# Kernel tuning notes

Measured on AMD Instinct MI355X. Metric: run time of the kernel, lower is better.

The kernel has to match this reference:

```python
import jax, jax.numpy as jnp
import numpy as np

B, L, D, K = 16, 2048, 768, 32
NEG = jnp.float32(-1e30)

def setup_inputs() -> dict:
    key = jax.random.key(0)
    k1, k2, k3, k4 = jax.random.split(key, 4)
    token_hidden = jax.random.normal(k1, (B, L, D), dtype=jnp.float32)
    attention_mask = jnp.ones((B, L), dtype=jnp.float32)
    # ragged spans: sorted boundaries -> contiguous, possibly-empty spans
    bounds = jnp.sort(jax.random.randint(k2, (B, K + 1), 0, L), axis=-1)
    span_starts = bounds[:, :-1].astype(jnp.int32)   # [B, K]
    span_ends = bounds[:, 1:].astype(jnp.int32)      # [B, K]
    w_pool = jax.random.normal(k3, (D,), dtype=jnp.float32) * 0.02
    b_pool = jax.random.normal(k4, (1,), dtype=jnp.float32) * 0.02
    return {"token_hidden": token_hidden, "attention_mask": attention_mask,
            "span_starts": span_starts, "span_ends": span_ends,
            "w_pool": w_pool, "b_pool": b_pool}

def reference(token_hidden, attention_mask, span_starts, span_ends, w_pool, b_pool):
    # sent_pool(vecs): scores per token, shared across spans  -> [B, L]
    scores = jnp.einsum('bld,d->bl', token_hidden, w_pool) + b_pool[0]
    pos = jnp.arange(token_hidden.shape[1], dtype=jnp.int32)  # [L]
    # span membership mask [B, K, L]; empty / out-of-range spans -> all False
    span_mask = ((pos[None, None, :] >= span_starts[:, :, None]) &
                 (pos[None, None, :] < span_ends[:, :, None]) &
                 (attention_mask[:, None, :] >= 0.5))
    logits = jnp.where(span_mask, scores[:, None, :], NEG)  # [B, K, L]
    m = jnp.max(logits, axis=-1, keepdims=True)
    e = jnp.exp(logits - m) * span_mask                      # stable masked softmax
    s = jnp.sum(e, axis=-1, keepdims=True)
    w = e / jnp.maximum(s, jnp.float32(1e-30))               # zero rows for empty spans
    H = jnp.einsum('bkl,bld->bkd', w, token_hidden)          # [B, K, D]
    sent_mask = jnp.any(span_mask, axis=-1).astype(jnp.float32)  # [B, K]
    return H, sent_mask
```

## Files before the change

### kernel.cpp

```cpp
#include <hip/hip_runtime.h>

#define BB 16
#define LL 2048
#define DD 768
#define KK 32
#define NEGI -1e30f

__global__ __launch_bounds__(256) void scores_k(
    const float* __restrict__ th,
    const float* __restrict__ attn,
    const float* __restrict__ wp,
    const float* __restrict__ bp,
    float* __restrict__ scores) {
  const int lane = threadIdx.x & 63;
  const int wave = threadIdx.x >> 6;
  const int token = (blockIdx.x << 2) + wave;

  const float4* row = (const float4*)(th + (size_t)token * DD);
  const float4* wr  = (const float4*)wp;

  float4 a0 = row[lane], a1 = row[lane + 64], a2 = row[lane + 128];
  float4 w0 = wr[lane],  w1 = wr[lane + 64],  w2 = wr[lane + 128];

  float acc = 0.f;
  acc = fmaf(a0.x, w0.x, acc); acc = fmaf(a0.y, w0.y, acc);
  acc = fmaf(a0.z, w0.z, acc); acc = fmaf(a0.w, w0.w, acc);
  acc = fmaf(a1.x, w1.x, acc); acc = fmaf(a1.y, w1.y, acc);
  acc = fmaf(a1.z, w1.z, acc); acc = fmaf(a1.w, w1.w, acc);
  acc = fmaf(a2.x, w2.x, acc); acc = fmaf(a2.y, w2.y, acc);
  acc = fmaf(a2.z, w2.z, acc); acc = fmaf(a2.w, w2.w, acc);

  #pragma unroll
  for (int o = 32; o > 0; o >>= 1) acc += __shfl_xor(acc, o, 64);

  if (lane == 0) {
    float s = acc + bp[0];
    scores[token] = (attn[token] >= 0.5f) ? s : NEGI;
  }
}

__global__ __launch_bounds__(64) void pool2_k(
    const float* __restrict__ th,
    const float* __restrict__ scores,
    const int* __restrict__ sps,
    const int* __restrict__ spe,
    float* __restrict__ Hout,
    float* __restrict__ sent) {
  const int bk = blockIdx.x;
  const int chunk = blockIdx.y;
  const int b = bk >> 5;
  const int lane = threadIdx.x;

  __shared__ float lw[LL];

  int s0 = min(max(sps[bk], 0), LL);
  int e0 = min(max(spe[bk], 0), LL);

  const float* sc = scores + (size_t)b * LL;

  float m = NEGI;
  for (int l = s0 + lane; l < e0; l += 64) m = fmaxf(m, sc[l]);
  #pragma unroll
  for (int o = 32; o > 0; o >>= 1) m = fmaxf(m, __shfl_xor(m, o, 64));

  float ss = 0.f;
  for (int l = s0 + lane; l < e0; l += 64) {
    float v = sc[l];
    ss += (v > -1e29f) ? __expf(v - m) : 0.f;
  }
  #pragma unroll
  for (int o = 32; o > 0; o >>= 1) ss += __shfl_xor(ss, o, 64);

  const float inv = (ss > 0.f) ? (1.0f / ss) : 0.f;

  for (int l = s0 + lane; l < e0; l += 64) {
    float v = sc[l];
    lw[l - s0] = (v > -1e29f) ? (__expf(v - m) * inv) : 0.f;
  }
  __syncthreads();

  const float4* base = (const float4*)(th + (size_t)b * LL * DD + chunk * 256) + lane;
  float4 acc = make_float4(0.f, 0.f, 0.f, 0.f);
  #pragma unroll 8
  for (int l = s0; l < e0; ++l) {
    const float w = lw[l - s0];
    float4 t = base[(size_t)l * (DD / 4)];
    acc.x = fmaf(w, t.x, acc.x);
    acc.y = fmaf(w, t.y, acc.y);
    acc.z = fmaf(w, t.z, acc.z);
    acc.w = fmaf(w, t.w, acc.w);
  }

  float4* o = (float4*)(Hout + (size_t)bk * DD + chunk * 256) + lane;
  *o = acc;

  if (chunk == 0 && lane == 0) sent[bk] = (ss > 0.f) ? 1.0f : 0.0f;
}

extern "C" void kernel_launch(void* const* d_in, const int* in_sizes, int n_in,
                              void* d_out, int out_size, void* d_ws, size_t ws_size,
                              hipStream_t stream) {
  const float* th   = (const float*)d_in[0];
  const float* attn = (const float*)d_in[1];
  const int*   sps  = (const int*)d_in[2];
  const int*   spe  = (const int*)d_in[3];
  const float* wp   = (const float*)d_in[4];
  const float* bp   = (const float*)d_in[5];

  float* Hout = (float*)d_out;
  float* sent = Hout + (size_t)BB * KK * DD;

  float* scores = (float*)d_ws;

  scores_k<<<dim3((BB * LL) / 4), dim3(256), 0, stream>>>(th, attn, wp, bp, scores);
  pool2_k<<<dim3(BB * KK, 3), dim3(64), 0, stream>>>(th, scores, sps, spe, Hout, sent);
}
```

Measured before the change: 174.5 us.

## Fuse score computation and span pooling into one online-softmax kernel

Merges the scoring kernel and the pooling kernel into a single per-span kernel. Sixteen waves each stream span rows, compute the dot-product score on the fly and keep an online-softmax running max, sum and weighted accumulator. The per-wave partials are then merged through shared memory. This removes the separate full pass over token_hidden to compute scores, plus the second launch and the workspace round trip. In exchange there are extra exp and rescale ops per token, only 512 blocks of 1024 threads, and load imbalance across uneven span lengths. The bias is dropped, which is valid because softmax is shift-invariant.

```diff
diff --git a/kernel.cpp b/kernel.cpp
--- a/kernel.cpp
+++ b/kernel.cpp
@@ -5,96 +5,94 @@
 #define DD 768
 #define KK 32
 #define NEGI -1e30f
+#define NW 16
 
-__global__ __launch_bounds__(256) void scores_k(
+__global__ __launch_bounds__(1024) void span_pool_k(
     const float* __restrict__ th,
     const float* __restrict__ attn,
-    const float* __restrict__ wp,
-    const float* __restrict__ bp,
-    float* __restrict__ scores) {
-  const int lane = threadIdx.x & 63;
-  const int wave = threadIdx.x >> 6;
-  const int token = (blockIdx.x << 2) + wave;
-
-  const float4* row = (const float4*)(th + (size_t)token * DD);
-  const float4* wr  = (const float4*)wp;
-
-  float4 a0 = row[lane], a1 = row[lane + 64], a2 = row[lane + 128];
-  float4 w0 = wr[lane],  w1 = wr[lane + 64],  w2 = wr[lane + 128];
-
-  float acc = 0.f;
-  acc = fmaf(a0.x, w0.x, acc); acc = fmaf(a0.y, w0.y, acc);
-  acc = fmaf(a0.z, w0.z, acc); acc = fmaf(a0.w, w0.w, acc);
-  acc = fmaf(a1.x, w1.x, acc); acc = fmaf(a1.y, w1.y, acc);
-  acc = fmaf(a1.z, w1.z, acc); acc = fmaf(a1.w, w1.w, acc);
-  acc = fmaf(a2.x, w2.x, acc); acc = fmaf(a2.y, w2.y, acc);
-  acc = fmaf(a2.z, w2.z, acc); acc = fmaf(a2.w, w2.w, acc);
-
-  #pragma unroll
-  for (int o = 32; o > 0; o >>= 1) acc += __shfl_xor(acc, o, 64);
-
-  if (lane == 0) {
-    float s = acc + bp[0];
-    scores[token] = (attn[token] >= 0.5f) ? s : NEGI;
-  }
-}
-
-__global__ __launch_bounds__(64) void pool2_k(
-    const float* __restrict__ th,
-    const float* __restrict__ scores,
     const int* __restrict__ sps,
     const int* __restrict__ spe,
+    const float* __restrict__ wp,
     float* __restrict__ Hout,
     float* __restrict__ sent) {
   const int bk = blockIdx.x;
-  const int chunk = blockIdx.y;
   const int b = bk >> 5;
-  const int lane = threadIdx.x;
+  const int lane = threadIdx.x & 63;
+  const int wave = threadIdx.x >> 6;
 
-  __shared__ float lw[LL];
+  __shared__ float sacc[NW][DD];
+  __shared__ float sm[NW], ssm[NW];
 
   int s0 = min(max(sps[bk], 0), LL);
   int e0 = min(max(spe[bk], 0), LL);
 
-  const float* sc = scores + (size_t)b * LL;
+  const float4* wr = (const float4*)wp;
+  const float4 w0 = wr[lane], w1 = wr[lane + 64], w2 = wr[lane + 128];
 
-  float m = NEGI;
-  for (int l = s0 + lane; l < e0; l += 64) m = fmaxf(m, sc[l]);
-  #pragma unroll
-  for (int o = 32; o > 0; o >>= 1) m = fmaxf(m, __shfl_xor(m, o, 64));
+  const float* arow = attn + (size_t)b * LL;
+  const float4* tb = (const float4*)(th + (size_t)b * LL * DD);
 
-  float ss = 0.f;
-  for (int l = s0 + lane; l < e0; l += 64) {
-    float v = sc[l];
-    ss += (v > -1e29f) ? __expf(v - m) : 0.f;
+  float m = NEGI, s = 0.f;
+  float4 a0 = make_float4(0.f, 0.f, 0.f, 0.f), a1 = a0, a2 = a0;
+
+  #pragma unroll 2
+  for (int l = s0 + wave; l < e0; l += NW) {
+    const float4* row = tb + (size_t)l * (DD / 4);
+    float4 r0 = row[lane], r1 = row[lane + 64], r2 = row[lane + 128];
+    float am = arow[l];
+
+    float d = 0.f;
+    d = fmaf(r0.x, w0.x, d); d = fmaf(r0.y, w0.y, d);
+    d = fmaf(r0.z, w0.z, d); d = fmaf(r0.w, w0.w, d);
+    d = fmaf(r1.x, w1.x, d); d = fmaf(r1.y, w1.y, d);
+    d = fmaf(r1.z, w1.z, d); d = fmaf(r1.w, w1.w, d);
+    d = fmaf(r2.x, w2.x, d); d = fmaf(r2.y, w2.y, d);
+    d = fmaf(r2.z, w2.z, d); d = fmaf(r2.w, w2.w, d);
+    #pragma unroll
+    for (int o = 32; o > 0; o >>= 1) d += __shfl_xor(d, o, 64);
+
+    if (am >= 0.5f) {
+      const float nm = fmaxf(m, d);
+      const float sc = __expf(m - nm);
+      const float e  = __expf(d - nm);
+      s = fmaf(s, sc, e);
+      a0.x = fmaf(e, r0.x, a0.x * sc); a0.y = fmaf(e, r0.y, a0.y * sc);
+      a0.z = fmaf(e, r0.z, a0.z * sc); a0.w = fmaf(e, r0.w, a0.w * sc);
+      a1.x = fmaf(e, r1.x, a1.x * sc); a1.y = fmaf(e, r1.y, a1.y * sc);
+      a1.z = fmaf(e, r1.z, a1.z * sc); a1.w = fmaf(e, r1.w, a1.w * sc);
+      a2.x = fmaf(e, r2.x, a2.x * sc); a2.y = fmaf(e, r2.y, a2.y * sc);
+      a2.z = fmaf(e, r2.z, a2.z * sc); a2.w = fmaf(e, r2.w, a2.w * sc);
+      m = nm;
+    }
   }
-  #pragma unroll
-  for (int o = 32; o > 0; o >>= 1) ss += __shfl_xor(ss, o, 64);
 
-  const float inv = (ss > 0.f) ? (1.0f / ss) : 0.f;
-
-  for (int l = s0 + lane; l < e0; l += 64) {
-    float v = sc[l];
-    lw[l - s0] = (v > -1e29f) ? (__expf(v - m) * inv) : 0.f;
-  }
+  float4* sa = (float4*)sacc[wave];
+  sa[lane] = a0; sa[lane + 64] = a1; sa[lane + 128] = a2;
+  if (lane == 0) { sm[wave] = m; ssm[wave] = s; }
   __syncthreads();
 
-  const float4* base = (const float4*)(th + (size_t)b * LL * DD + chunk * 256) + lane;
-  float4 acc = make_float4(0.f, 0.f, 0.f, 0.f);
-  #pragma unroll 8
-  for (int l = s0; l < e0; ++l) {
-    const float w = lw[l - s0];
-    float4 t = base[(size_t)l * (DD / 4)];
-    acc.x = fmaf(w, t.x, acc.x);
-    acc.y = fmaf(w, t.y, acc.y);
-    acc.z = fmaf(w, t.z, acc.z);
-    acc.w = fmaf(w, t.w, acc.w);
+  const int t = threadIdx.x;
+  if (t < DD / 4) {
+    float M = NEGI;
+    #pragma unroll
+    for (int w = 0; w < NW; ++w) M = fmaxf(M, sm[w]);
+    float S = 0.f;
+    #pragma unroll
+    for (int w = 0; w < NW; ++w) S = fmaf(__expf(sm[w] - M), ssm[w], S);
+    const float inv = (S > 0.f) ? (1.0f / S) : 0.f;
+
+    float4 o = make_float4(0.f, 0.f, 0.f, 0.f);
+    #pragma unroll
+    for (int w = 0; w < NW; ++w) {
+      const float ew = __expf(sm[w] - M);
+      const float4 p = ((const float4*)sacc[w])[t];
+      o.x = fmaf(ew, p.x, o.x); o.y = fmaf(ew, p.y, o.y);
+      o.z = fmaf(ew, p.z, o.z); o.w = fmaf(ew, p.w, o.w);
+    }
+    o.x *= inv; o.y *= inv; o.z *= inv; o.w *= inv;
+    ((float4*)(Hout + (size_t)bk * DD))[t] = o;
+    if (t == 0) sent[bk] = (S > 0.f) ? 1.0f : 0.0f;
   }
-
-  float4* o = (float4*)(Hout + (size_t)bk * DD + chunk * 256) + lane;
-  *o = acc;
-
-  if (chunk == 0 && lane == 0) sent[bk] = (ss > 0.f) ? 1.0f : 0.0f;
 }
 
 extern "C" void kernel_launch(void* const* d_in, const int* in_sizes, int n_in,
@@ -105,13 +103,10 @@
   const int*   sps  = (const int*)d_in[2];
   const int*   spe  = (const int*)d_in[3];
   const float* wp   = (const float*)d_in[4];
-  const float* bp   = (const float*)d_in[5];
 
   float* Hout = (float*)d_out;
   float* sent = Hout + (size_t)BB * KK * DD;
 
-  float* scores = (float*)d_ws;
-
-  scores_k<<<dim3((BB * LL) / 4), dim3(256), 0, stream>>>(th, attn, wp, bp, scores);
-  pool2_k<<<dim3(BB * KK, 3), dim3(64), 0, stream>>>(th, scores, sps, spe, Hout, sent);
+  span_pool_k<<<dim3(BB * KK), dim3(1024), 0, stream>>>(
+      th, attn, sps, spe, wp, Hout, sent);
 }
```

After: 167.9 us. -3.8%, faster.
